# Kernel tuning notes

Measured on AMD Instinct MI355X. Metric: run time of the kernel, lower is better.

The kernel has to match this reference:

```python
import jax, jax.numpy as jnp
import numpy as np
import math

COARSE_K = 20
FINE_K = 10
KNOWLEDGE_RANK = 128


def setup_inputs() -> dict:
    key = jax.random.key(0)
    ks = jax.random.split(key, 5)
    B, S, D = 2, 2048, 1024
    NK = 65536
    return {
        "x": jax.random.normal(ks[0], (B, S, D), dtype=jnp.float32),
        "W_router": jax.random.normal(ks[1], (D, NK), dtype=jnp.float32) * 0.02,
        "W_enc": jax.random.normal(ks[2], (D, KNOWLEDGE_RANK), dtype=jnp.float32) * 0.02,
        "K_all": jax.random.normal(ks[3], (NK, KNOWLEDGE_RANK), dtype=jnp.float32) * 0.02,
        "V_all": jax.random.normal(ks[4], (NK, D), dtype=jnp.float32) * 0.02,
    }


def reference(x, W_router, W_enc, K_all, V_all):
    # Stage 1: coarse routing over full knowledge table
    k_logits = jnp.einsum('bsd,dn->bsn', x, W_router)          # [B,S,NK]
    coarse_scores, candidate_idx = jax.lax.top_k(k_logits, COARSE_K)  # [B,S,Ck]

    # Stage 2: fine scoring against gathered coarse candidates
    query = jnp.einsum('bsd,dr->bsr', x, W_enc)                # [B,S,R]
    K_candidates = K_all[candidate_idx]                        # [B,S,Ck,R]
    fine_scores = jnp.einsum('bsr,bscr->bsc', query, K_candidates) / math.sqrt(KNOWLEDGE_RANK)

    fine_topk_scores, fine_local_idx = jax.lax.top_k(fine_scores, FINE_K)  # [B,S,Fk]
    fine_weights = jax.nn.softmax(fine_topk_scores, axis=-1)
    fine_global_idx = jnp.take_along_axis(candidate_idx, fine_local_idx, axis=-1)  # [B,S,Fk]

    selected_V = V_all[fine_global_idx]                        # [B,S,Fk,D]
    output = jnp.einsum('bsfd,bsf->bsd', selected_V, fine_weights)
    return output
```

## Files before the change

### kernel.cpp

```cpp
#include <hip/hip_runtime.h>

#define DIM 1024
#define NKN 65536
#define TOK 4096
#define CK 20
#define FK 10
#define RNK 128
#define CAP 256
#define NCHUNK 512

typedef __bf16 v8bf __attribute__((ext_vector_type(8)));
typedef float v4f __attribute__((ext_vector_type(4)));

#define AS1 __attribute__((address_space(1)))
#define AS3 __attribute__((address_space(3)))

__device__ __forceinline__ unsigned short f2bf(float f) {
  unsigned u = __builtin_bit_cast(unsigned, f);
  u += 0x7FFFu + ((u >> 16) & 1u);
  return (unsigned short)(u >> 16);
}
__device__ __forceinline__ unsigned short bf2key(unsigned short b) {
  return (b & 0x8000) ? (unsigned short)(~b) : (unsigned short)(b | 0x8000);
}

__global__ __launch_bounds__(256) void k_transpose(const float* __restrict__ W,
                                                   float* __restrict__ WT,
                                                   unsigned short* __restrict__ WTb) {
  __shared__ float tile[32][33];
  const int n0 = (blockIdx.x & 2047) << 5;
  const int d0 = (blockIdx.x >> 11) << 5;
  const int c = threadIdx.x & 31, r0 = threadIdx.x >> 5;
#pragma unroll
  for (int i = 0; i < 4; i++) {
    int r = r0 + i * 8;
    tile[r][c] = W[(size_t)(d0 + r) * NKN + n0 + c];
  }
  __syncthreads();
#pragma unroll
  for (int i = 0; i < 4; i++) {
    int r = r0 + i * 8;
    float v = tile[c][r];
    size_t o = (size_t)(n0 + r) * DIM + d0 + c;
    WT[o] = v;
    WTb[o] = f2bf(v);
  }
}

__global__ __launch_bounds__(256) void k_cvt_x(const float* __restrict__ x,
                                               unsigned short* __restrict__ xb) {
  const int i = blockIdx.x * 256 + threadIdx.x;
  const float4 v = reinterpret_cast<const float4*>(x)[i];
  ushort4 o;
  o.x = f2bf(v.x); o.y = f2bf(v.y); o.z = f2bf(v.z); o.w = f2bf(v.w);
  reinterpret_cast<ushort4*>(xb)[i] = o;
}

__global__ __launch_bounds__(512, 4) void k_gemm(const unsigned short* __restrict__ A,
                                                 const unsigned short* __restrict__ Bt,
                                                 unsigned* __restrict__ Ttop) {
  __shared__ __align__(16) char lds[73728];
  const int tid = threadIdx.x;
  const int lane = tid & 63, wid = tid >> 6;
  const int wm = wid >> 1, wn = wid & 1;
  const int mb = blockIdx.x & 15, nb = blockIdx.x >> 4;
  const int m0 = mb << 8, n0 = nb << 7;
  const int rm = lane & 15, lq = lane >> 4;
  v4f acc[4][4] = {};

  const int u8 = (((tid & 3) ^ ((tid >> 3) & 3)) << 3);
  const unsigned short* aSrc = A + (size_t)(m0 + (tid >> 2)) * DIM + u8;
  const unsigned short* bSrc = Bt + (size_t)(n0 + (tid >> 2)) * DIM + u8;

  const int sx = ((lq ^ ((rm >> 1) & 3)) << 4);
  const int aOff = (wm * 64 + rm) * 64 + sx;
  const int bOff = 16384 + (wn * 64 + rm) * 64 + sx;

#define STAGE(SLOT, KT) do { \
    char* _b = lds + (SLOT) * 24576 + tid * 16; \
    __builtin_amdgcn_global_load_lds((const AS1 void*)(aSrc + (KT)),             (AS3 void*)(_b),         16, 0, 0); \
    __builtin_amdgcn_global_load_lds((const AS1 void*)(aSrc + (KT) + 128 * DIM), (AS3 void*)(_b + 8192),  16, 0, 0); \
    __builtin_amdgcn_global_load_lds((const AS1 void*)(bSrc + (KT)),             (AS3 void*)(_b + 16384), 16, 0, 0); \
  } while (0)

#define TILE(T, VM, DOSTAGE) do { \
    asm volatile("s_waitcnt vmcnt(" VM ")" ::: "memory"); \
    __builtin_amdgcn_s_barrier(); \
    if (DOSTAGE) STAGE(((T) + 2) % 3, ((T) + 2) * 32); \
    const char* sb = lds + ((T) % 3) * 24576; \
    v8bf a0 = *(const v8bf*)(sb + aOff); \
    v8bf a1 = *(const v8bf*)(sb + aOff + 1024); \
    v8bf a2 = *(const v8bf*)(sb + aOff + 2048); \
    v8bf a3 = *(const v8bf*)(sb + aOff + 3072); \
    v8bf b0 = *(const v8bf*)(sb + bOff); \
    v8bf b1 = *(const v8bf*)(sb + bOff + 1024); \
    v8bf b2 = *(const v8bf*)(sb + bOff + 2048); \
    v8bf b3 = *(const v8bf*)(sb + bOff + 3072); \
    __builtin_amdgcn_s_setprio(1); \
    _Pragma("unroll") for (int nf = 0; nf < 4; ++nf) { \
      v8bf bb = (nf == 0) ? b0 : (nf == 1) ? b1 : (nf == 2) ? b2 : b3; \
      acc[0][nf] = __builtin_amdgcn_mfma_f32_16x16x32_bf16(a0, bb, acc[0][nf], 0, 0, 0); \
      acc[1][nf] = __builtin_amdgcn_mfma_f32_16x16x32_bf16(a1, bb, acc[1][nf], 0, 0, 0); \
      acc[2][nf] = __builtin_amdgcn_mfma_f32_16x16x32_bf16(a2, bb, acc[2][nf], 0, 0, 0); \
      acc[3][nf] = __builtin_amdgcn_mfma_f32_16x16x32_bf16(a3, bb, acc[3][nf], 0, 0, 0); \
    } \
    __builtin_amdgcn_s_setprio(0); \
  } while (0)

  STAGE(0, 0);
  STAGE(1, 32);

  for (int t = 0; t < 30; ++t) {
    TILE(t, "3", true);
  }
  TILE(30, "3", false);
  TILE(31, "0", false);
#undef TILE
#undef STAGE

  __syncthreads();
  unsigned short* keys = (unsigned short*)lds;
#pragma unroll
  for (int fr = 0; fr < 4; ++fr) {
    const int lrow = wm * 64 + fr * 16 + lq * 4;
#pragma unroll
    for (int nf = 0; nf < 4; ++nf) {
      const int lcol = wn * 64 + nf * 16 + rm;
#pragma unroll
      for (int r = 0; r < 4; ++r)
        keys[(lrow + r) * 136 + lcol] = bf2key(f2bf(acc[fr][nf][r]));
    }
  }
  __syncthreads();
  if (tid < 256) {
    const uint4* krow = (const uint4*)((const char*)lds + tid * 272);
    unsigned s0 = 0, s1 = 0, s2 = 0, s3 = 0, s4 = 0, s5 = 0, s6 = 0, s7 = 0;
#pragma unroll 4
    for (int k = 0; k < 16; ++k) {
      const uint4 wv = krow[k];
      const unsigned base = (unsigned)(n0 + k * 8);
      const unsigned wd[4] = {wv.x, wv.y, wv.z, wv.w};
#pragma unroll
      for (int q = 0; q < 4; ++q) {
        const unsigned c0 = ((wd[q] & 0xFFFFu) << 16) | (base + 2 * q);
        const unsigned c1 = (wd[q] & 0xFFFF0000u) | (base + 2 * q + 1);
#define INS(C) \
        if ((C) > s7) { \
          s7 = (C); unsigned tswp; \
          if (s7 > s6) { tswp = s6; s6 = s7; s7 = tswp; } \
          if (s6 > s5) { tswp = s5; s5 = s6; s6 = tswp; } \
          if (s5 > s4) { tswp = s4; s4 = s5; s5 = tswp; } \
          if (s4 > s3) { tswp = s3; s3 = s4; s4 = tswp; } \
          if (s3 > s2) { tswp = s2; s2 = s3; s3 = tswp; } \
          if (s2 > s1) { tswp = s1; s1 = s2; s2 = tswp; } \
          if (s1 > s0) { tswp = s0; s0 = s1; s1 = tswp; } \
        }
        INS(c0)
        INS(c1)
#undef INS
      }
    }
    unsigned* dst = Ttop + ((size_t)(m0 + tid) * NCHUNK + nb) * 8;
    uint4 o0 = {s0, s1, s2, s3}, o1 = {s4, s5, s6, s7};
    reinterpret_cast<uint4*>(dst)[0] = o0;
    reinterpret_cast<uint4*>(dst)[1] = o1;
  }
}

__global__ __launch_bounds__(256) void k_pickscore(const unsigned* __restrict__ Ttop,
                                                   const float* __restrict__ x,
                                                   const float* __restrict__ WT,
                                                   int* __restrict__ coarse) {
  __shared__ unsigned ent[NCHUNK * 8];
  __shared__ __align__(16) float xs[DIM];
  __shared__ double sc[CAP];
  __shared__ int ci[CAP];
  __shared__ int scnt, bsS;
  const int t = blockIdx.x, tid = threadIdx.x;
  const int lane = tid & 63, w = tid >> 6;
  {
    const uint4* src = reinterpret_cast<const uint4*>(Ttop + (size_t)t * NCHUNK * 8);
    for (int i = tid; i < 1024; i += 256)
      reinterpret_cast<uint4*>(ent)[i] = src[i];
    reinterpret_cast<float4*>(xs)[tid] =
        reinterpret_cast<const float4*>(x + (size_t)t * DIM)[tid];
  }
  if (tid == 0) scnt = 0;
  __syncthreads();
  if (w == 0) {
    int v[8];
#pragma unroll
    for (int j = 0; j < 8; j++) v[j] = (int)(ent[(lane * 8 + j) * 8] >> 16);
    int t32 = 0;
    for (int it = 0; it < 32; it++) {
      int lm = v[0];
#pragma unroll
      for (int j = 1; j < 8; j++) lm = max(lm, v[j]);
      int gm = lm;
#pragma unroll
      for (int off = 32; off > 0; off >>= 1) gm = max(gm, __shfl_xor(gm, off));
      unsigned long long msk = __ballot(lm == gm);
      if (lane == __ffsll((long long)msk) - 1) {
        bool done = false;
#pragma unroll
        for (int j = 0; j < 8; j++)
          if (!done && v[j] == gm) { v[j] = -1; done = true; }
      }
      t32 = gm;
    }
    if (lane == 0) bsS = t32;
  }
  __syncthreads();
  const unsigned bs = (unsigned)bsS;
  for (int i = tid; i < NCHUNK * 8; i += 256) {
    const unsigned e = ent[i];
    if ((e >> 16) >= bs) {
      int p = atomicAdd(&scnt, 1);
      if (p < CAP) ci[p] = (int)(e & 0xFFFFu);
    }
  }
  __syncthreads();
  const int cnt = min(scnt, CAP);
  if (tid < CAP) {
    if (tid >= cnt) ci[tid] = 0;
    sc[tid] = -1e300;
  }
  __syncthreads();
  for (int c = w; c < cnt; c += 4) {
    const float4* wr = reinterpret_cast<const float4*>(WT + (size_t)ci[c] * DIM);
    const float4* xv4 = reinterpret_cast<const float4*>(xs);
    double sacc = 0.0;
#pragma unroll
    for (int k = 0; k < 4; k++) {
      float4 wv = wr[k * 64 + lane];
      float4 xv = xv4[k * 64 + lane];
      sacc += (double)xv.x * wv.x + (double)xv.y * wv.y
            + (double)xv.z * wv.z + (double)xv.w * wv.w;
    }
#pragma unroll
    for (int off = 32; off > 0; off >>= 1) sacc += __shfl_down(sacc, off);
    if (lane == 0) sc[c] = sacc;
  }
  __syncthreads();
  if (w == 0) {
    double v[4];
    int ix[4];
#pragma unroll
    for (int j = 0; j < 4; j++) { v[j] = sc[lane + j * 64]; ix[j] = lane + j * 64; }
    for (int kk = 0; kk < CK; kk++) {
      double v1 = v[0]; int i1 = ix[0];
#pragma unroll
      for (int j = 1; j < 4; j++)
        if (v[j] > v1) { v1 = v[j]; i1 = ix[j]; }
#pragma unroll
      for (int off = 32; off > 0; off >>= 1) {
        double ov = __shfl_down(v1, off);
        int oi = __shfl_down(i1, off);
        if (ov > v1) { v1 = ov; i1 = oi; }
      }
      i1 = __shfl(i1, 0);
      if (lane == 0) coarse[(size_t)t * CK + kk] = ci[i1];
#pragma unroll
      for (int j = 0; j < 4; j++)
        if (i1 == ix[j]) v[j] = -1e300;
    }
  }
}

__global__ __launch_bounds__(256) void k_fine(const float* __restrict__ x,
                                              const float* __restrict__ Wenc,
                                              const float* __restrict__ Kall,
                                              const float* __restrict__ Vall,
                                              const int* __restrict__ coarse,
                                              float* __restrict__ out) {
  __shared__ float xs[DIM];
  __shared__ float pq[2][RNK];
  __shared__ float qs[RNK];
  __shared__ float fsc[CK];
  __shared__ int gix[CK];
  __shared__ float wts[FK];
  __shared__ int fidx[FK];
  const int t = blockIdx.x, tid = threadIdx.x;
  const int lane = tid & 63, w = tid >> 6;
  reinterpret_cast<float4*>(xs)[tid] = reinterpret_cast<const float4*>(x + (size_t)t * DIM)[tid];
  if (tid < CK) gix[tid] = coarse[(size_t)t * CK + tid];
  __syncthreads();
  {
    const int j = tid & 127, half = tid >> 7;
    float s = 0.f;
    const int d0 = half * 512;
#pragma unroll 8
    for (int d = 0; d < 512; d++)
      s = fmaf(xs[d0 + d], Wenc[(size_t)(d0 + d) * RNK + j], s);
    pq[half][j] = s;
  }
  __syncthreads();
  if (tid < RNK) qs[tid] = pq[0][tid] + pq[1][tid];
  __syncthreads();
  for (int c = w; c < CK; c += 4) {
    const float* kr = Kall + (size_t)gix[c] * RNK;
    float s = 0.f;
    s = fmaf(qs[lane], kr[lane], s);
    s = fmaf(qs[lane + 64], kr[lane + 64], s);
#pragma unroll
    for (int off = 32; off > 0; off >>= 1) s += __shfl_down(s, off);
    if (lane == 0) fsc[c] = s * 0.08838834764831843f;
  }
  __syncthreads();
  if (w == 0) {
    float vv = (lane < CK) ? fsc[lane] : -3e38f;
    float myv = -3e38f; int myp = 0;
    for (int kk = 0; kk < FK; kk++) {
      float v1 = vv; int p1 = lane;
#pragma unroll
      for (int off = 32; off > 0; off >>= 1) {
        float ov = __shfl_down(v1, off);
        int op = __shfl_down(p1, off);
        if (ov > v1) { v1 = ov; p1 = op; }
      }
      v1 = __shfl(v1, 0); p1 = __shfl(p1, 0);
      if (lane == kk) { myv = v1; myp = p1; }
      if (lane == p1) vv = -3e38f;
    }
    float sv = (lane < FK) ? myv : -3e38f;
    float mx = sv;
#pragma unroll
    for (int off = 8; off > 0; off >>= 1) mx = fmaxf(mx, __shfl_xor(mx, off, 16));
    float e = (lane < FK) ? expf(sv - mx) : 0.f;
    float se = e;
#pragma unroll
    for (int off = 8; off > 0; off >>= 1) se += __shfl_xor(se, off, 16);
    if (lane < FK) { wts[lane] = e / se; fidx[lane] = gix[myp]; }
  }
  __syncthreads();
  float4 a = make_float4(0.f, 0.f, 0.f, 0.f);
#pragma unroll
  for (int f = 0; f < FK; f++) {
    const float wt = wts[f];
    const float4 v = *reinterpret_cast<const float4*>(&Vall[(size_t)fidx[f] * DIM + tid * 4]);
    a.x = fmaf(wt, v.x, a.x);
    a.y = fmaf(wt, v.y, a.y);
    a.z = fmaf(wt, v.z, a.z);
    a.w = fmaf(wt, v.w, a.w);
  }
  *reinterpret_cast<float4*>(&out[(size_t)t * DIM + tid * 4]) = a;
}


extern "C" void kernel_launch(void* const* d_in, const int* in_sizes, int n_in,
                              void* d_out, int out_size, void* d_ws, size_t ws_size,
                              hipStream_t stream) {
  const float* x = (const float*)d_in[0];
  const float* Wr = (const float*)d_in[1];
  const float* Wenc = (const float*)d_in[2];
  const float* Kall = (const float*)d_in[3];
  const float* Vall = (const float*)d_in[4];
  float* out = (float*)d_out;

  char* ws = (char*)d_ws;
  constexpr size_t OFF_WT = 0;
  constexpr size_t OFF_WTB = 268435456;
  constexpr size_t OFF_XB = 402653184;
  constexpr size_t OFF_TTOP = 411041792;
  float* WT = (float*)(ws + OFF_WT);
  unsigned short* WTb = (unsigned short*)(ws + OFF_WTB);
  unsigned short* xb = (unsigned short*)(ws + OFF_XB);
  unsigned* Ttop = (unsigned*)(ws + OFF_TTOP);
  int* coarse = (int*)(ws + OFF_XB);

  k_transpose<<<65536, 256, 0, stream>>>(Wr, WT, WTb);
  k_cvt_x<<<4096, 256, 0, stream>>>(x, xb);
  k_gemm<<<8192, 512, 0, stream>>>(xb, WTb, Ttop);
  k_pickscore<<<4096, 256, 0, stream>>>(Ttop, x, WT, coarse);
  k_fine<<<4096, 256, 0, stream>>>(x, Wenc, Kall, Vall, coarse, out);
}
```

Before: 985.9 us.

## Batch query projection over 8 tokens and pair rescoring loads per wave

The query projection x·W_enc moves out of the per-token fine kernel into a separate kernel. That kernel handles 8 tokens per block, so each W_enc element loaded is reused across 8 tokens instead of being re-read 4096 times. Separately, the fp64 rescoring loop in k_pickscore now processes two candidates per wave iteration to give more memory-level parallelism. This adds one kernel launch and a query buffer in the workspace, and the 8-token block needs 32KB of LDS.

```diff
diff --git a/kernel.cpp b/kernel.cpp
--- a/kernel.cpp
+++ b/kernel.cpp
@@ -226,20 +226,34 @@
     sc[tid] = -1e300;
   }
   __syncthreads();
-  for (int c = w; c < cnt; c += 4) {
-    const float4* wr = reinterpret_cast<const float4*>(WT + (size_t)ci[c] * DIM);
+  {
     const float4* xv4 = reinterpret_cast<const float4*>(xs);
-    double sacc = 0.0;
-#pragma unroll
-    for (int k = 0; k < 4; k++) {
-      float4 wv = wr[k * 64 + lane];
-      float4 xv = xv4[k * 64 + lane];
-      sacc += (double)xv.x * wv.x + (double)xv.y * wv.y
-            + (double)xv.z * wv.z + (double)xv.w * wv.w;
-    }
-#pragma unroll
-    for (int off = 32; off > 0; off >>= 1) sacc += __shfl_down(sacc, off);
-    if (lane == 0) sc[c] = sacc;
+    for (int c = w; c < cnt; c += 8) {
+      const int c2 = c + 4;
+      const bool has2 = (c2 < cnt);
+      const float4* wr1 = reinterpret_cast<const float4*>(WT + (size_t)ci[c] * DIM);
+      const float4* wr2 = reinterpret_cast<const float4*>(WT + (size_t)ci[has2 ? c2 : c] * DIM);
+      double sa = 0.0, sb2 = 0.0;
+#pragma unroll
+      for (int k = 0; k < 4; k++) {
+        const float4 w1 = wr1[k * 64 + lane];
+        const float4 w2 = wr2[k * 64 + lane];
+        const float4 xv = xv4[k * 64 + lane];
+        sa  += (double)xv.x * w1.x + (double)xv.y * w1.y
+             + (double)xv.z * w1.z + (double)xv.w * w1.w;
+        sb2 += (double)xv.x * w2.x + (double)xv.y * w2.y
+             + (double)xv.z * w2.z + (double)xv.w * w2.w;
+      }
+#pragma unroll
+      for (int off = 32; off > 0; off >>= 1) {
+        sa += __shfl_down(sa, off);
+        sb2 += __shfl_down(sb2, off);
+      }
+      if (lane == 0) {
+        sc[c] = sa;
+        if (has2) sc[c2] = sb2;
+      }
+    }
   }
   __syncthreads();
   if (w == 0) {
@@ -267,14 +281,38 @@
   }
 }
 
-__global__ __launch_bounds__(256) void k_fine(const float* __restrict__ x,
-                                              const float* __restrict__ Wenc,
+__global__ __launch_bounds__(256) void k_query8(const float* __restrict__ x,
+                                                const float* __restrict__ Wenc,
+                                                float* __restrict__ q) {
+  __shared__ __align__(16) float xs8[8 * DIM];
+  __shared__ float pq[2][8][RNK];
+  const int t0 = blockIdx.x * 8, tid = threadIdx.x;
+  for (int i = tid; i < 2048; i += 256)
+    reinterpret_cast<float4*>(xs8)[i] =
+        reinterpret_cast<const float4*>(x + (size_t)t0 * DIM)[i];
+  __syncthreads();
+  const int j = tid & 127, g = tid >> 7;
+  float s[8] = {0.f, 0.f, 0.f, 0.f, 0.f, 0.f, 0.f, 0.f};
+  for (int d = g * 512; d < g * 512 + 512; ++d) {
+    const float wv = Wenc[(size_t)d * RNK + j];
+#pragma unroll
+    for (int tok = 0; tok < 8; ++tok)
+      s[tok] = fmaf(xs8[tok * DIM + d], wv, s[tok]);
+  }
+#pragma unroll
+  for (int tok = 0; tok < 8; ++tok) pq[g][tok][j] = s[tok];
+  __syncthreads();
+  for (int i = tid; i < 8 * RNK; i += 256) {
+    const int tok = i >> 7, jj = i & 127;
+    q[(size_t)(t0 + tok) * RNK + jj] = pq[0][tok][jj] + pq[1][tok][jj];
+  }
+}
+
+__global__ __launch_bounds__(256) void k_fine(const float* __restrict__ q,
                                               const float* __restrict__ Kall,
                                               const float* __restrict__ Vall,
                                               const int* __restrict__ coarse,
                                               float* __restrict__ out) {
-  __shared__ float xs[DIM];
-  __shared__ float pq[2][RNK];
   __shared__ float qs[RNK];
   __shared__ float fsc[CK];
   __shared__ int gix[CK];
@@ -282,20 +320,8 @@
   __shared__ int fidx[FK];
   const int t = blockIdx.x, tid = threadIdx.x;
   const int lane = tid & 63, w = tid >> 6;
-  reinterpret_cast<float4*>(xs)[tid] = reinterpret_cast<const float4*>(x + (size_t)t * DIM)[tid];
+  if (tid < RNK) qs[tid] = q[(size_t)t * RNK + tid];
   if (tid < CK) gix[tid] = coarse[(size_t)t * CK + tid];
-  __syncthreads();
-  {
-    const int j = tid & 127, half = tid >> 7;
-    float s = 0.f;
-    const int d0 = half * 512;
-#pragma unroll 8
-    for (int d = 0; d < 512; d++)
-      s = fmaf(xs[d0 + d], Wenc[(size_t)(d0 + d) * RNK + j], s);
-    pq[half][j] = s;
-  }
-  __syncthreads();
-  if (tid < RNK) qs[tid] = pq[0][tid] + pq[1][tid];
   __syncthreads();
   for (int c = w; c < CK; c += 4) {
     const float* kr = Kall + (size_t)gix[c] * RNK;
@@ -367,10 +393,12 @@
   unsigned short* xb = (unsigned short*)(ws + OFF_XB);
   unsigned* Ttop = (unsigned*)(ws + OFF_TTOP);
   int* coarse = (int*)(ws + OFF_XB);
+  float* q = (float*)(ws + OFF_XB + 4194304);
 
   k_transpose<<<65536, 256, 0, stream>>>(Wr, WT, WTb);
   k_cvt_x<<<4096, 256, 0, stream>>>(x, xb);
   k_gemm<<<8192, 512, 0, stream>>>(xb, WTb, Ttop);
   k_pickscore<<<4096, 256, 0, stream>>>(Ttop, x, WT, coarse);
-  k_fine<<<4096, 256, 0, stream>>>(x, Wenc, Kall, Vall, coarse, out);
-}
+  k_query8<<<512, 256, 0, stream>>>(x, Wenc, q);
+  k_fine<<<4096, 256, 0, stream>>>(q, Kall, Vall, coarse, out);
+}
```

Measured after the change: 972.5 us. About the same (-1.4%).
